# Performance work log

Measured on AMD Instinct MI355X. Metric: run time of the kernel, lower is better.

Reference implementation:

```python
import jax, jax.numpy as jnp
import numpy as np

H = 512  # hidden_dim


def setup_inputs() -> dict:
    key = jax.random.key(0)
    ks = jax.random.split(key, 9)
    B, T, TGT = 512, 512, 28
    s = 1.0 / np.sqrt(H)
    return {
        "sequence": jax.random.normal(ks[0], (B, T, 1), dtype=jnp.float32),
        "W_ih": jax.random.normal(ks[1], (4 * H, 1), dtype=jnp.float32) * s,
        "W_hh": jax.random.normal(ks[2], (4 * H, H), dtype=jnp.float32) * s,
        "b_ih": jax.random.normal(ks[3], (4 * H,), dtype=jnp.float32) * s,
        "b_hh": jax.random.normal(ks[4], (4 * H,), dtype=jnp.float32) * s,
        "fc1_w": jax.random.normal(ks[5], (H // 2, H), dtype=jnp.float32) * s,
        "fc1_b": jax.random.normal(ks[6], (H // 2,), dtype=jnp.float32) * s,
        "fc2_w": jax.random.normal(ks[7], (TGT, H // 2), dtype=jnp.float32) * (1.0 / np.sqrt(H // 2)),
        "fc2_b": jax.random.normal(ks[8], (TGT,), dtype=jnp.float32) * (1.0 / np.sqrt(H // 2)),
    }


def reference(sequence, W_ih, W_hh, b_ih, b_hh, fc1_w, fc1_b, fc2_w, fc2_b):
    B = sequence.shape[0]
    # Precompute input projections for all timesteps: [B,T,1] @ [1,4H] -> [T,B,4H]
    x_proj = jnp.einsum('bti,gi->tbg', sequence, W_ih) + b_ih + b_hh  # fold both biases

    def step(carry, xp):
        h, c = carry
        gates = xp + h @ W_hh.T                      # [B,4H]
        i, f, g, o = jnp.split(gates, 4, axis=-1)    # PyTorch LSTMCell gate order
        i = jax.nn.sigmoid(i)
        f = jax.nn.sigmoid(f)
        g = jnp.tanh(g)
        o = jax.nn.sigmoid(o)
        c_new = f * c + i * g
        h_new = o * jnp.tanh(c_new)
        return (h_new, c_new), None

    h0 = jnp.zeros((B, H), dtype=sequence.dtype)
    (h, _), _ = jax.lax.scan(step, (h0, h0), x_proj)

    # MLP head: Linear -> ReLU -> Linear, then unsqueeze to [B, target, 1]
    z = jax.nn.relu(h @ fc1_w.T + fc1_b)
    out = z @ fc2_w.T + fc2_b
    return out[:, :, None]
```

## Files before the change

kernel.cpp:

```cpp
#include <hip/hip_runtime.h>
#include <math.h>

#define H   512
#define B   512
#define T   512
#define TGT 28

typedef __bf16 bf16x8 __attribute__((ext_vector_type(8)));
typedef float  f32x4  __attribute__((ext_vector_type(4)));
typedef unsigned short u16;

#define OFF_WPH  0x000000u
#define OFF_WPL  0x200000u
#define OFF_HHI0 0x400000u
#define OFF_HLO0 0x480000u
#define OFF_SYNC 0x500000u
#define OFF_HHI1 0x501000u
#define OFF_HLO1 0x581000u

#define SMEM_BYTES 131072

__device__ inline u16 f2bf(float x) {
    unsigned u = __builtin_bit_cast(unsigned, x);
    u += 0x7FFFu + ((u >> 16) & 1u);
    return (u16)(u >> 16);
}
__device__ inline float bf2f(u16 h) {
    unsigned u = ((unsigned)h) << 16;
    return __builtin_bit_cast(float, u);
}
__device__ inline float frcp(float x) {
    float r = __builtin_amdgcn_rcpf(x);
    return r * fmaf(-x, r, 2.0f);
}
__device__ inline float fsig(float x) {
    return frcp(1.0f + __expf(-x));
}
__device__ inline float ftanh(float x) {
    return fmaf(2.0f, fsig(2.0f * x), -1.0f);
}

__device__ inline void group_barrier(int* gb, int kh, int l, int seq) {
    if (l == 0)
        __hip_atomic_store(&gb[kh], seq, __ATOMIC_RELEASE,
                           __HIP_MEMORY_SCOPE_WORKGROUP);
    int guard = 0;
    for (;;) {
        int v = __hip_atomic_load(&gb[l & 3], __ATOMIC_ACQUIRE,
                                  __HIP_MEMORY_SCOPE_WORKGROUP);
        if (__all(v >= seq)) break;
        if (++guard > (1 << 17)) break;
    }
}

__global__ __launch_bounds__(256) void init_pack(const float* __restrict__ Whh,
                                                 u16* __restrict__ wph,
                                                 u16* __restrict__ wpl) {
    int idx = blockIdx.x * 256 + threadIdx.x;
    int l  = idx & 63;
    int S  = (idx >> 6) & 15;
    int q  = (idx >> 10) & 3;
    int r  = idx >> 12;
    int g  = q * 512 + r * 16 + (l & 15);
    int k  = S * 32 + ((l >> 4) * 8);
    const float* src = Whh + (size_t)g * H + k;
    __align__(16) u16 hi8[8];
    __align__(16) u16 lo8[8];
#pragma unroll
    for (int j = 0; j < 8; ++j) {
        float w = src[j];
        u16 hb = f2bf(w);
        hi8[j] = hb;
        lo8[j] = f2bf(w - bf2f(hb));
    }
    *(uint4*)(wph + (size_t)idx * 8) = *(const uint4*)hi8;
    *(uint4*)(wpl + (size_t)idx * 8) = *(const uint4*)lo8;
}

__global__ __launch_bounds__(256) void init_state(unsigned* __restrict__ zbase) {
    int idx = blockIdx.x * 256 + threadIdx.x;
    if (idx < 263168) zbase[idx] = 0u;
}

__global__ __launch_bounds__(512, 1) void lstm_persistent(
    const u16* __restrict__ wph, const u16* __restrict__ wpl,
    u16* __restrict__ hhi0, u16* __restrict__ hlo0,
    u16* __restrict__ hhi1, u16* __restrict__ hlo1,
    int* __restrict__ sync, const float* __restrict__ seq,
    const float* __restrict__ Wih, const float* __restrict__ bih,
    const float* __restrict__ bhh)
{
    extern __shared__ char smem[];
    u16* wh = (u16*)smem;
    u16* wl = wh + 32768;
    __shared__ __align__(16) float gatesT[2][64][36];
    __shared__ int gbar[2][4];
    __shared__ int grel[2];
    __shared__ int sh_pr[2];

    const int tid = threadIdx.x;
    const int l   = tid & 63;
    const int w   = tid >> 6;
    const int g   = w >> 2;
    const int kh  = w & 3;

    if (tid == 0) {
        unsigned xcc;
        asm volatile("s_getreg_b32 %0, hwreg(HW_REG_XCC_ID)" : "=s"(xcc));
        int p = (int)(xcc & 7u);
        int r = __hip_atomic_fetch_add(&sync[p * 32], 1,
                                       __ATOMIC_RELAXED, __HIP_MEMORY_SCOPE_AGENT);
        sh_pr[0] = p;
        sh_pr[1] = r & 31;
    }
    if (tid < 8) gbar[tid >> 2][tid & 3] = 0;
    if (tid < 2) grel[tid] = 0;
    __syncthreads();
    const int p = sh_pr[0];
    const int r = sh_pr[1];
    int* arrp = &sync[256 + p * 64 + g * 32];
    int* gb   = gbar[g];

    {
        const uint4* gh = (const uint4*)(wph + (size_t)r * 32768);
        const uint4* gl = (const uint4*)(wpl + (size_t)r * 32768);
        uint4* sh = (uint4*)wh;
        uint4* sl = (uint4*)wl;
#pragma unroll
        for (int i = 0; i < 8; ++i) {
            int idx = tid + i * 512;
            sh[idx] = gh[idx];
            sl[idx] = gl[idx];
        }
    }

    const int lt   = tid & 255;
    const int cc   = lt & 15;
    const int m0   = lt >> 4;
    const int kcol = r * 16 + cc;
    float wib[4], bb[4];
#pragma unroll
    for (int q = 0; q < 4; ++q) {
        int gg = q * 512 + kcol;
        wib[q] = Wih[gg];
        bb[q]  = bih[gg] + bhh[gg];
    }
    float cr0 = 0.0f, cr1 = 0.0f;
    const int pb = p * 64;
    const int b0 = pb + g * 32 + m0;
    const int b1 = b0 + 16;

    const int arow0 = (pb + g * 32 + (l & 15)) * H;
    const int arow1 = arow0 + 16 * H;

    __syncthreads();

    for (int t = 0; t < T; ++t) {
        const u16* hih = (t & 1) ? hhi1 : hhi0;
        const u16* hil = (t & 1) ? hlo1 : hlo0;
        u16* hoh = (t & 1) ? hhi0 : hhi1;
        u16* hol = (t & 1) ? hlo0 : hlo1;

        float sv0 = seq[(size_t)b0 * T + t];
        float sv1 = seq[(size_t)b1 * T + t];

        f32x4 acc[2][4] = {};

#pragma unroll 1
        for (int s = 0; s < 4; ++s) {
            const int S  = kh * 4 + s;
            const int ka = S * 32 + ((l >> 4) * 8);
            bf16x8 a0h = *(const bf16x8*)(hih + arow0 + ka);
            bf16x8 a1h = *(const bf16x8*)(hih + arow1 + ka);
            bf16x8 a0l = *(const bf16x8*)(hil + arow0 + ka);
            bf16x8 a1l = *(const bf16x8*)(hil + arow1 + ka);
#pragma unroll
            for (int n = 0; n < 4; ++n) {
                const int fo = ((n * 16 + S) * 64 + l) * 8;
                bf16x8 bh = *(const bf16x8*)(wh + fo);
                bf16x8 bl = *(const bf16x8*)(wl + fo);
                acc[0][n] = __builtin_amdgcn_mfma_f32_16x16x32_bf16(a0h, bh, acc[0][n], 0, 0, 0);
                acc[1][n] = __builtin_amdgcn_mfma_f32_16x16x32_bf16(a1h, bh, acc[1][n], 0, 0, 0);
                acc[0][n] = __builtin_amdgcn_mfma_f32_16x16x32_bf16(a0h, bl, acc[0][n], 0, 0, 0);
                acc[1][n] = __builtin_amdgcn_mfma_f32_16x16x32_bf16(a1h, bl, acc[1][n], 0, 0, 0);
                acc[0][n] = __builtin_amdgcn_mfma_f32_16x16x32_bf16(a0l, bh, acc[0][n], 0, 0, 0);
                acc[1][n] = __builtin_amdgcn_mfma_f32_16x16x32_bf16(a1l, bh, acc[1][n], 0, 0, 0);
            }
        }

        const int base = t * 5;
#pragma unroll
        for (int rr = 0; rr < 4; ++rr) {
            if (kh == rr) {
#pragma unroll
                for (int ms = 0; ms < 2; ++ms)
#pragma unroll
                    for (int n = 0; n < 4; ++n) {
                        const int n2 = n * 16 + (l & 15);
                        const int mb = ms * 16 + ((l >> 4) << 2);
                        float* gp = &gatesT[g][n2][mb];
                        if (rr == 0) {
                            *(f32x4*)gp = acc[ms][n];
                        } else {
                            f32x4 v = *(const f32x4*)gp;
                            v += acc[ms][n];
                            *(f32x4*)gp = v;
                        }
                    }
            }
            group_barrier(gb, kh, l, base + rr + 1);
        }

        {
            float pre[4];
#pragma unroll
            for (int q = 0; q < 4; ++q) pre[q] = gatesT[g][q * 16 + cc][m0] + fmaf(sv0, wib[q], bb[q]);
            float ig = fsig(pre[0]);
            float fg = fsig(pre[1]);
            float gg2 = ftanh(pre[2]);
            float og = fsig(pre[3]);
            cr0 = fg * cr0 + ig * gg2;
            float hv = og * ftanh(cr0);
            u16 hb = f2bf(hv);
            size_t ci = (size_t)b0 * H + kcol;
            hoh[ci] = hb;
            hol[ci] = f2bf(hv - bf2f(hb));
        }
        {
            float pre[4];
#pragma unroll
            for (int q = 0; q < 4; ++q) pre[q] = gatesT[g][q * 16 + cc][m0 + 16] + fmaf(sv1, wib[q], bb[q]);
            float ig = fsig(pre[0]);
            float fg = fsig(pre[1]);
            float gg2 = ftanh(pre[2]);
            float og = fsig(pre[3]);
            cr1 = fg * cr1 + ig * gg2;
            float hv = og * ftanh(cr1);
            u16 hb = f2bf(hv);
            size_t ci = (size_t)b1 * H + kcol;
            hoh[ci] = hb;
            hol[ci] = f2bf(hv - bf2f(hb));
        }

        if (t < T - 1) {
            asm volatile("s_waitcnt vmcnt(0)" ::: "memory");
            group_barrier(gb, kh, l, base + 5);
            if (kh == 0 && l == 0) {
                __hip_atomic_fetch_add(arrp, 1, __ATOMIC_RELAXED,
                                       __HIP_MEMORY_SCOPE_AGENT);
                const int target = 32 * (t + 1);
                int guard = 0;
                while (__hip_atomic_load(arrp, __ATOMIC_RELAXED,
                                         __HIP_MEMORY_SCOPE_AGENT) < target) {
                    __builtin_amdgcn_s_sleep(1);
                    if (++guard > (1 << 18)) break;
                }
                __hip_atomic_store(&grel[g], t + 1, __ATOMIC_RELEASE,
                                   __HIP_MEMORY_SCOPE_WORKGROUP);
            }
            {
                int guard = 0;
                while (__hip_atomic_load(&grel[g], __ATOMIC_ACQUIRE,
                                         __HIP_MEMORY_SCOPE_WORKGROUP) < t + 1) {
                    if (++guard > (1 << 17)) break;
                }
            }
            asm volatile("buffer_inv sc0" ::: "memory");
        }
    }
}

__global__ __launch_bounds__(256) void head_kernel(const u16* __restrict__ hhi,
                                                   const u16* __restrict__ hlo,
                                                   const float* __restrict__ fc1w,
                                                   const float* __restrict__ fc1b,
                                                   const float* __restrict__ fc2w,
                                                   const float* __restrict__ fc2b,
                                                   float* __restrict__ out) {
    const int b = blockIdx.x;
    const int tid = threadIdx.x;
    __shared__ __align__(16) float hb[H];
    __shared__ float z[256];

    hb[tid]       = bf2f(hhi[(size_t)b * H + tid])       + bf2f(hlo[(size_t)b * H + tid]);
    hb[tid + 256] = bf2f(hhi[(size_t)b * H + tid + 256]) + bf2f(hlo[(size_t)b * H + tid + 256]);
    __syncthreads();

    float acc = fc1b[tid];
    const float4* wr = (const float4*)(fc1w + (size_t)tid * H);
    const float4* hr = (const float4*)hb;
#pragma unroll 4
    for (int kk = 0; kk < H / 4; ++kk) {
        float4 wv = wr[kk], hv = hr[kk];
        acc += wv.x * hv.x + wv.y * hv.y + wv.z * hv.z + wv.w * hv.w;
    }
    z[tid] = fmaxf(acc, 0.0f);
    __syncthreads();

    if (tid < TGT) {
        float a = fc2b[tid];
        const float* w2 = fc2w + (size_t)tid * 256;
#pragma unroll 8
        for (int j = 0; j < 256; ++j) a += z[j] * w2[j];
        out[(size_t)b * TGT + tid] = a;
    }
}

extern "C" void kernel_launch(void* const* d_in, const int* in_sizes, int n_in,
                              void* d_out, int out_size, void* d_ws, size_t ws_size,
                              hipStream_t stream) {
    const float* seq  = (const float*)d_in[0];
    const float* Wih  = (const float*)d_in[1];
    const float* Whh  = (const float*)d_in[2];
    const float* bih  = (const float*)d_in[3];
    const float* bhh  = (const float*)d_in[4];
    const float* fc1w = (const float*)d_in[5];
    const float* fc1b = (const float*)d_in[6];
    const float* fc2w = (const float*)d_in[7];
    const float* fc2b = (const float*)d_in[8];
    float* out = (float*)d_out;

    char* wsb = (char*)d_ws;
    u16* wph  = (u16*)(wsb + OFF_WPH);
    u16* wpl  = (u16*)(wsb + OFF_WPL);
    u16* hhi0 = (u16*)(wsb + OFF_HHI0);
    u16* hlo0 = (u16*)(wsb + OFF_HLO0);
    u16* hhi1 = (u16*)(wsb + OFF_HHI1);
    u16* hlo1 = (u16*)(wsb + OFF_HLO1);
    int* sync = (int*)(wsb + OFF_SYNC);

    init_pack<<<512, 256, 0, stream>>>(Whh, wph, wpl);
    init_state<<<1028, 256, 0, stream>>>((unsigned*)(wsb + OFF_HHI0));

    hipFuncSetAttribute((const void*)lstm_persistent,
                        hipFuncAttributeMaxDynamicSharedMemorySize, SMEM_BYTES);

    void* args[] = {(void*)&wph, (void*)&wpl, (void*)&hhi0, (void*)&hlo0,
                    (void*)&hhi1, (void*)&hlo1, (void*)&sync, (void*)&seq,
                    (void*)&Wih, (void*)&bih, (void*)&bhh};
    hipLaunchCooperativeKernel((const void*)lstm_persistent, dim3(256), dim3(512),
                               args, SMEM_BYTES, stream);

    head_kernel<<<B, 256, 0, stream>>>(hhi0, hlo0, fc1w, fc1b, fc2w, fc2b, out);
}
```

Measured before the change: 4.181 ms.

## Regroup warps into four batch groups with two-way K split

Warps are reorganized from 2 batch groups of 32 rows, each with a 4-way K split, into 4 groups of 16 rows, each with a 2-way K split. The per-step reduction of partial gates in shared memory drops from four serialized accumulate phases with 5 group barriers to two phases with 3 barriers. This shortens the serial sync chain inside each recurrent step. In exchange, each weight fragment read from LDS feeds only one row tile instead of two, so LDS weight traffic per warp doubles. The global cross-block arrival counters are re-indexed for the four groups.

New measurement: 12.35 ms. 195% more time.

```diff
diff --git a/kernel.cpp b/kernel.cpp
--- a/kernel.cpp
+++ b/kernel.cpp
@@ -40,13 +40,13 @@
     return fmaf(2.0f, fsig(2.0f * x), -1.0f);
 }
 
-__device__ inline void group_barrier(int* gb, int kh, int l, int seq) {
+__device__ inline void group_barrier2(int* gb, int kk, int l, int seq) {
     if (l == 0)
-        __hip_atomic_store(&gb[kh], seq, __ATOMIC_RELEASE,
+        __hip_atomic_store(&gb[kk], seq, __ATOMIC_RELEASE,
                            __HIP_MEMORY_SCOPE_WORKGROUP);
     int guard = 0;
     for (;;) {
-        int v = __hip_atomic_load(&gb[l & 3], __ATOMIC_ACQUIRE,
+        int v = __hip_atomic_load(&gb[l & 1], __ATOMIC_ACQUIRE,
                                   __HIP_MEMORY_SCOPE_WORKGROUP);
         if (__all(v >= seq)) break;
         if (++guard > (1 << 17)) break;
@@ -93,16 +93,16 @@
     extern __shared__ char smem[];
     u16* wh = (u16*)smem;
     u16* wl = wh + 32768;
-    __shared__ __align__(16) float gatesT[2][64][36];
-    __shared__ int gbar[2][4];
-    __shared__ int grel[2];
+    __shared__ __align__(16) float gatesT[4][64][20];
+    __shared__ int gbar[4][2];
+    __shared__ int grel[4];
     __shared__ int sh_pr[2];
 
     const int tid = threadIdx.x;
     const int l   = tid & 63;
     const int w   = tid >> 6;
-    const int g   = w >> 2;
-    const int kh  = w & 3;
+    const int g   = w >> 1;
+    const int kk  = w & 1;
 
     if (tid == 0) {
         unsigned xcc;
@@ -113,12 +113,12 @@
         sh_pr[0] = p;
         sh_pr[1] = r & 31;
     }
-    if (tid < 8) gbar[tid >> 2][tid & 3] = 0;
-    if (tid < 2) grel[tid] = 0;
+    if (tid < 8) gbar[tid >> 1][tid & 1] = 0;
+    if (tid < 4) grel[tid] = 0;
     __syncthreads();
     const int p = sh_pr[0];
     const int r = sh_pr[1];
-    int* arrp = &sync[256 + p * 64 + g * 32];
+    int* arrp = &sync[256 + p * 64 + g * 16];
     int* gb   = gbar[g];
 
     {
@@ -134,7 +134,7 @@
         }
     }
 
-    const int lt   = tid & 255;
+    const int lt   = tid & 127;
     const int cc   = lt & 15;
     const int m0   = lt >> 4;
     const int kcol = r * 16 + cc;
@@ -147,11 +147,10 @@
     }
     float cr0 = 0.0f, cr1 = 0.0f;
     const int pb = p * 64;
-    const int b0 = pb + g * 32 + m0;
-    const int b1 = b0 + 16;
-
-    const int arow0 = (pb + g * 32 + (l & 15)) * H;
-    const int arow1 = arow0 + 16 * H;
+    const int b0 = pb + g * 16 + m0;
+    const int b1 = b0 + 8;
+
+    const int arow0 = (pb + g * 16 + (l & 15)) * H;
 
     __syncthreads();
 
@@ -164,52 +163,47 @@
         float sv0 = seq[(size_t)b0 * T + t];
         float sv1 = seq[(size_t)b1 * T + t];
 
-        f32x4 acc[2][4] = {};
+        f32x4 acc[4] = {};
 
 #pragma unroll 1
-        for (int s = 0; s < 4; ++s) {
-            const int S  = kh * 4 + s;
+        for (int s = 0; s < 8; ++s) {
+            const int S  = kk * 8 + s;
             const int ka = S * 32 + ((l >> 4) * 8);
-            bf16x8 a0h = *(const bf16x8*)(hih + arow0 + ka);
-            bf16x8 a1h = *(const bf16x8*)(hih + arow1 + ka);
-            bf16x8 a0l = *(const bf16x8*)(hil + arow0 + ka);
-            bf16x8 a1l = *(const bf16x8*)(hil + arow1 + ka);
+            bf16x8 ah = *(const bf16x8*)(hih + arow0 + ka);
+            bf16x8 al = *(const bf16x8*)(hil + arow0 + ka);
 #pragma unroll
             for (int n = 0; n < 4; ++n) {
                 const int fo = ((n * 16 + S) * 64 + l) * 8;
                 bf16x8 bh = *(const bf16x8*)(wh + fo);
                 bf16x8 bl = *(const bf16x8*)(wl + fo);
-                acc[0][n] = __builtin_amdgcn_mfma_f32_16x16x32_bf16(a0h, bh, acc[0][n], 0, 0, 0);
-                acc[1][n] = __builtin_amdgcn_mfma_f32_16x16x32_bf16(a1h, bh, acc[1][n], 0, 0, 0);
-                acc[0][n] = __builtin_amdgcn_mfma_f32_16x16x32_bf16(a0h, bl, acc[0][n], 0, 0, 0);
-                acc[1][n] = __builtin_amdgcn_mfma_f32_16x16x32_bf16(a1h, bl, acc[1][n], 0, 0, 0);
-                acc[0][n] = __builtin_amdgcn_mfma_f32_16x16x32_bf16(a0l, bh, acc[0][n], 0, 0, 0);
-                acc[1][n] = __builtin_amdgcn_mfma_f32_16x16x32_bf16(a1l, bh, acc[1][n], 0, 0, 0);
-            }
-        }
-
-        const int base = t * 5;
-#pragma unroll
-        for (int rr = 0; rr < 4; ++rr) {
-            if (kh == rr) {
-#pragma unroll
-                for (int ms = 0; ms < 2; ++ms)
-#pragma unroll
-                    for (int n = 0; n < 4; ++n) {
-                        const int n2 = n * 16 + (l & 15);
-                        const int mb = ms * 16 + ((l >> 4) << 2);
-                        float* gp = &gatesT[g][n2][mb];
-                        if (rr == 0) {
-                            *(f32x4*)gp = acc[ms][n];
-                        } else {
-                            f32x4 v = *(const f32x4*)gp;
-                            v += acc[ms][n];
-                            *(f32x4*)gp = v;
-                        }
-                    }
-            }
-            group_barrier(gb, kh, l, base + rr + 1);
-        }
+                acc[n] = __builtin_amdgcn_mfma_f32_16x16x32_bf16(ah, bh, acc[n], 0, 0, 0);
+                acc[n] = __builtin_amdgcn_mfma_f32_16x16x32_bf16(ah, bl, acc[n], 0, 0, 0);
+                acc[n] = __builtin_amdgcn_mfma_f32_16x16x32_bf16(al, bh, acc[n], 0, 0, 0);
+            }
+        }
+
+        const int base = t * 3;
+        if (kk == 0) {
+#pragma unroll
+            for (int n = 0; n < 4; ++n) {
+                const int n2 = n * 16 + (l & 15);
+                const int mb = (l >> 4) << 2;
+                *(f32x4*)&gatesT[g][n2][mb] = acc[n];
+            }
+        }
+        group_barrier2(gb, kk, l, base + 1);
+        if (kk == 1) {
+#pragma unroll
+            for (int n = 0; n < 4; ++n) {
+                const int n2 = n * 16 + (l & 15);
+                const int mb = (l >> 4) << 2;
+                float* gp = &gatesT[g][n2][mb];
+                f32x4 v = *(const f32x4*)gp;
+                v += acc[n];
+                *(f32x4*)gp = v;
+            }
+        }
+        group_barrier2(gb, kk, l, base + 2);
 
         {
             float pre[4];
@@ -229,7 +223,7 @@
         {
             float pre[4];
 #pragma unroll
-            for (int q = 0; q < 4; ++q) pre[q] = gatesT[g][q * 16 + cc][m0 + 16] + fmaf(sv1, wib[q], bb[q]);
+            for (int q = 0; q < 4; ++q) pre[q] = gatesT[g][q * 16 + cc][m0 + 8] + fmaf(sv1, wib[q], bb[q]);
             float ig = fsig(pre[0]);
             float fg = fsig(pre[1]);
             float gg2 = ftanh(pre[2]);
@@ -244,8 +238,8 @@
 
         if (t < T - 1) {
             asm volatile("s_waitcnt vmcnt(0)" ::: "memory");
-            group_barrier(gb, kh, l, base + 5);
-            if (kh == 0 && l == 0) {
+            group_barrier2(gb, kk, l, base + 3);
+            if (kk == 0 && l == 0) {
                 __hip_atomic_fetch_add(arrp, 1, __ATOMIC_RELAXED,
                                        __HIP_MEMORY_SCOPE_AGENT);
                 const int target = 32 * (t + 1);
```

## Read low weight half from global, halve gate-reduction barriers, add sleep in spin

Applied to the files above, without the earlier changes.

Only the high bf16 half of the recurrent weights is staged into LDS. The low half is now read from global memory (L2/L1) on every timestep, which halves dynamic shared memory. The four-way sequential gate reduction over k-slices is replaced by two accumulation buffers written in pairs, cutting per-step group barriers from five to three. The intra-block spin wait also gets an s_sleep to reduce contention. The tradeoff is that global loads inside the MFMA inner loop may add latency on every step.

New measurement: 5.007 ms. +19.8%, slower.

```diff
diff --git a/kernel.cpp b/kernel.cpp
--- a/kernel.cpp
+++ b/kernel.cpp
@@ -18,7 +18,7 @@
 #define OFF_HHI1 0x501000u
 #define OFF_HLO1 0x581000u
 
-#define SMEM_BYTES 131072
+#define SMEM_BYTES 65536
 
 __device__ inline u16 f2bf(float x) {
     unsigned u = __builtin_bit_cast(unsigned, x);
@@ -92,8 +92,8 @@
 {
     extern __shared__ char smem[];
     u16* wh = (u16*)smem;
-    u16* wl = wh + 32768;
-    __shared__ __align__(16) float gatesT[2][64][36];
+    __shared__ __align__(16) float gA[2][64][36];
+    __shared__ __align__(16) float gB[2][64][36];
     __shared__ int gbar[2][4];
     __shared__ int grel[2];
     __shared__ int sh_pr[2];
@@ -123,16 +123,14 @@
 
     {
         const uint4* gh = (const uint4*)(wph + (size_t)r * 32768);
-        const uint4* gl = (const uint4*)(wpl + (size_t)r * 32768);
         uint4* sh = (uint4*)wh;
-        uint4* sl = (uint4*)wl;
 #pragma unroll
         for (int i = 0; i < 8; ++i) {
             int idx = tid + i * 512;
             sh[idx] = gh[idx];
-            sl[idx] = gl[idx];
-        }
-    }
+        }
+    }
+    const u16* glo = wpl + (size_t)r * 32768;
 
     const int lt   = tid & 255;
     const int cc   = lt & 15;
@@ -178,7 +176,7 @@
             for (int n = 0; n < 4; ++n) {
                 const int fo = ((n * 16 + S) * 64 + l) * 8;
                 bf16x8 bh = *(const bf16x8*)(wh + fo);
-                bf16x8 bl = *(const bf16x8*)(wl + fo);
+                bf16x8 bl = *(const bf16x8*)(glo + fo);
                 acc[0][n] = __builtin_amdgcn_mfma_f32_16x16x32_bf16(a0h, bh, acc[0][n], 0, 0, 0);
                 acc[1][n] = __builtin_amdgcn_mfma_f32_16x16x32_bf16(a1h, bh, acc[1][n], 0, 0, 0);
                 acc[0][n] = __builtin_amdgcn_mfma_f32_16x16x32_bf16(a0h, bl, acc[0][n], 0, 0, 0);
@@ -188,33 +186,41 @@
             }
         }
 
-        const int base = t * 5;
-#pragma unroll
-        for (int rr = 0; rr < 4; ++rr) {
-            if (kh == rr) {
-#pragma unroll
-                for (int ms = 0; ms < 2; ++ms)
-#pragma unroll
-                    for (int n = 0; n < 4; ++n) {
-                        const int n2 = n * 16 + (l & 15);
-                        const int mb = ms * 16 + ((l >> 4) << 2);
-                        float* gp = &gatesT[g][n2][mb];
-                        if (rr == 0) {
-                            *(f32x4*)gp = acc[ms][n];
-                        } else {
-                            f32x4 v = *(const f32x4*)gp;
-                            v += acc[ms][n];
-                            *(f32x4*)gp = v;
-                        }
-                    }
-            }
-            group_barrier(gb, kh, l, base + rr + 1);
-        }
+        const int base = t * 3;
+        if (kh == 0 || kh == 2) {
+            float (*gt)[36] = (kh == 0) ? gA[g] : gB[g];
+#pragma unroll
+            for (int ms = 0; ms < 2; ++ms)
+#pragma unroll
+                for (int n = 0; n < 4; ++n) {
+                    const int n2 = n * 16 + (l & 15);
+                    const int mb = ms * 16 + ((l >> 4) << 2);
+                    *(f32x4*)&gt[n2][mb] = acc[ms][n];
+                }
+        }
+        group_barrier(gb, kh, l, base + 1);
+        if (kh == 1 || kh == 3) {
+            float (*gt)[36] = (kh == 1) ? gA[g] : gB[g];
+#pragma unroll
+            for (int ms = 0; ms < 2; ++ms)
+#pragma unroll
+                for (int n = 0; n < 4; ++n) {
+                    const int n2 = n * 16 + (l & 15);
+                    const int mb = ms * 16 + ((l >> 4) << 2);
+                    float* gp = &gt[n2][mb];
+                    f32x4 v = *(const f32x4*)gp;
+                    v += acc[ms][n];
+                    *(f32x4*)gp = v;
+                }
+        }
+        group_barrier(gb, kh, l, base + 2);
 
         {
             float pre[4];
 #pragma unroll
-            for (int q = 0; q < 4; ++q) pre[q] = gatesT[g][q * 16 + cc][m0] + fmaf(sv0, wib[q], bb[q]);
+            for (int q = 0; q < 4; ++q)
+                pre[q] = gA[g][q * 16 + cc][m0] + gB[g][q * 16 + cc][m0]
+                       + fmaf(sv0, wib[q], bb[q]);
             float ig = fsig(pre[0]);
             float fg = fsig(pre[1]);
             float gg2 = ftanh(pre[2]);
@@ -229,7 +235,9 @@
         {
             float pre[4];
 #pragma unroll
-            for (int q = 0; q < 4; ++q) pre[q] = gatesT[g][q * 16 + cc][m0 + 16] + fmaf(sv1, wib[q], bb[q]);
+            for (int q = 0; q < 4; ++q)
+                pre[q] = gA[g][q * 16 + cc][m0 + 16] + gB[g][q * 16 + cc][m0 + 16]
+                       + fmaf(sv1, wib[q], bb[q]);
             float ig = fsig(pre[0]);
             float fg = fsig(pre[1]);
             float gg2 = ftanh(pre[2]);
@@ -244,7 +252,7 @@
 
         if (t < T - 1) {
             asm volatile("s_waitcnt vmcnt(0)" ::: "memory");
-            group_barrier(gb, kh, l, base + 5);
+            group_barrier(gb, kh, l, base + 3);
             if (kh == 0 && l == 0) {
                 __hip_atomic_fetch_add(arrp, 1, __ATOMIC_RELAXED,
                                        __HIP_MEMORY_SCOPE_AGENT);
@@ -262,7 +270,8 @@
                 int guard = 0;
                 while (__hip_atomic_load(&grel[g], __ATOMIC_ACQUIRE,
                                          __HIP_MEMORY_SCOPE_WORKGROUP) < t + 1) {
-                    if (++guard > (1 << 17)) break;
+                    __builtin_amdgcn_s_sleep(2);
+                    if (++guard > (1 << 16)) break;
                 }
             }
             asm volatile("buffer_inv sc0" ::: "memory");
```

## Split LSTM gate GEMM across waves by K-half and N-half to cut reduction barriers

Applied to the files above, without the earlier changes.

Each of the four waves in a batch group previously computed all four N-tiles over one quarter of K, then reduced through shared memory in four serialized barrier rounds. Now waves split work two ways in K and two ways in N, so the reduction needs only two barrier rounds per timestep. Each wave now loads the A fragments over twice as many K steps, adding some global reads of h. Spin-wait guard limits are also lowered, which risks breaking out early if a barrier wait runs long.

New measurement: 5.756 ms. 1.38x slower.

```diff
diff --git a/kernel.cpp b/kernel.cpp
--- a/kernel.cpp
+++ b/kernel.cpp
@@ -40,16 +40,16 @@
     return fmaf(2.0f, fsig(2.0f * x), -1.0f);
 }
 
-__device__ inline void group_barrier(int* gb, int kh, int l, int seq) {
+__device__ inline void group_barrier(int* gb, int wq, int l, int seq) {
     if (l == 0)
-        __hip_atomic_store(&gb[kh], seq, __ATOMIC_RELEASE,
+        __hip_atomic_store(&gb[wq], seq, __ATOMIC_RELEASE,
                            __HIP_MEMORY_SCOPE_WORKGROUP);
     int guard = 0;
     for (;;) {
         int v = __hip_atomic_load(&gb[l & 3], __ATOMIC_ACQUIRE,
                                   __HIP_MEMORY_SCOPE_WORKGROUP);
         if (__all(v >= seq)) break;
-        if (++guard > (1 << 17)) break;
+        if (++guard > (1 << 14)) break;
     }
 }
 
@@ -102,7 +102,9 @@
     const int l   = tid & 63;
     const int w   = tid >> 6;
     const int g   = w >> 2;
-    const int kh  = w & 3;
+    const int wq  = w & 3;
+    const int kk  = wq & 1;
+    const int nn  = wq >> 1;
 
     if (tid == 0) {
         unsigned xcc;
@@ -164,52 +166,57 @@
         float sv0 = seq[(size_t)b0 * T + t];
         float sv1 = seq[(size_t)b1 * T + t];
 
-        f32x4 acc[2][4] = {};
+        f32x4 acc[2][2] = {};
 
 #pragma unroll 1
-        for (int s = 0; s < 4; ++s) {
-            const int S  = kh * 4 + s;
+        for (int s = 0; s < 8; ++s) {
+            const int S  = kk * 8 + s;
             const int ka = S * 32 + ((l >> 4) * 8);
             bf16x8 a0h = *(const bf16x8*)(hih + arow0 + ka);
             bf16x8 a1h = *(const bf16x8*)(hih + arow1 + ka);
             bf16x8 a0l = *(const bf16x8*)(hil + arow0 + ka);
             bf16x8 a1l = *(const bf16x8*)(hil + arow1 + ka);
 #pragma unroll
-            for (int n = 0; n < 4; ++n) {
+            for (int j = 0; j < 2; ++j) {
+                const int n  = nn * 2 + j;
                 const int fo = ((n * 16 + S) * 64 + l) * 8;
                 bf16x8 bh = *(const bf16x8*)(wh + fo);
                 bf16x8 bl = *(const bf16x8*)(wl + fo);
-                acc[0][n] = __builtin_amdgcn_mfma_f32_16x16x32_bf16(a0h, bh, acc[0][n], 0, 0, 0);
-                acc[1][n] = __builtin_amdgcn_mfma_f32_16x16x32_bf16(a1h, bh, acc[1][n], 0, 0, 0);
-                acc[0][n] = __builtin_amdgcn_mfma_f32_16x16x32_bf16(a0h, bl, acc[0][n], 0, 0, 0);
-                acc[1][n] = __builtin_amdgcn_mfma_f32_16x16x32_bf16(a1h, bl, acc[1][n], 0, 0, 0);
-                acc[0][n] = __builtin_amdgcn_mfma_f32_16x16x32_bf16(a0l, bh, acc[0][n], 0, 0, 0);
-                acc[1][n] = __builtin_amdgcn_mfma_f32_16x16x32_bf16(a1l, bh, acc[1][n], 0, 0, 0);
+                acc[0][j] = __builtin_amdgcn_mfma_f32_16x16x32_bf16(a0h, bh, acc[0][j], 0, 0, 0);
+                acc[1][j] = __builtin_amdgcn_mfma_f32_16x16x32_bf16(a1h, bh, acc[1][j], 0, 0, 0);
+                acc[0][j] = __builtin_amdgcn_mfma_f32_16x16x32_bf16(a0h, bl, acc[0][j], 0, 0, 0);
+                acc[1][j] = __builtin_amdgcn_mfma_f32_16x16x32_bf16(a1h, bl, acc[1][j], 0, 0, 0);
+                acc[0][j] = __builtin_amdgcn_mfma_f32_16x16x32_bf16(a0l, bh, acc[0][j], 0, 0, 0);
+                acc[1][j] = __builtin_amdgcn_mfma_f32_16x16x32_bf16(a1l, bh, acc[1][j], 0, 0, 0);
             }
         }
 
-        const int base = t * 5;
-#pragma unroll
-        for (int rr = 0; rr < 4; ++rr) {
-            if (kh == rr) {
-#pragma unroll
-                for (int ms = 0; ms < 2; ++ms)
-#pragma unroll
-                    for (int n = 0; n < 4; ++n) {
-                        const int n2 = n * 16 + (l & 15);
-                        const int mb = ms * 16 + ((l >> 4) << 2);
-                        float* gp = &gatesT[g][n2][mb];
-                        if (rr == 0) {
-                            *(f32x4*)gp = acc[ms][n];
-                        } else {
-                            f32x4 v = *(const f32x4*)gp;
-                            v += acc[ms][n];
-                            *(f32x4*)gp = v;
-                        }
-                    }
-            }
-            group_barrier(gb, kh, l, base + rr + 1);
-        }
+        const int base = t * 3;
+        if (kk == 0) {
+#pragma unroll
+            for (int ms = 0; ms < 2; ++ms)
+#pragma unroll
+                for (int j = 0; j < 2; ++j) {
+                    const int n2 = (nn * 2 + j) * 16 + (l & 15);
+                    const int mb = ms * 16 + ((l >> 4) << 2);
+                    *(f32x4*)&gatesT[g][n2][mb] = acc[ms][j];
+                }
+        }
+        group_barrier(gb, wq, l, base + 1);
+        if (kk == 1) {
+#pragma unroll
+            for (int ms = 0; ms < 2; ++ms)
+#pragma unroll
+                for (int j = 0; j < 2; ++j) {
+                    const int n2 = (nn * 2 + j) * 16 + (l & 15);
+                    const int mb = ms * 16 + ((l >> 4) << 2);
+                    float* gp = &gatesT[g][n2][mb];
+                    f32x4 v = *(const f32x4*)gp;
+                    v += acc[ms][j];
+                    *(f32x4*)gp = v;
+                }
+        }
+        group_barrier(gb, wq, l, base + 2);
 
         {
             float pre[4];
@@ -244,8 +251,8 @@
 
         if (t < T - 1) {
             asm volatile("s_waitcnt vmcnt(0)" ::: "memory");
-            group_barrier(gb, kh, l, base + 5);
-            if (kh == 0 && l == 0) {
+            group_barrier(gb, wq, l, base + 3);
+            if (wq == 0 && l == 0) {
                 __hip_atomic_fetch_add(arrp, 1, __ATOMIC_RELAXED,
                                        __HIP_MEMORY_SCOPE_AGENT);
                 const int target = 32 * (t + 1);
@@ -253,7 +260,7 @@
                 while (__hip_atomic_load(arrp, __ATOMIC_RELAXED,
                                          __HIP_MEMORY_SCOPE_AGENT) < target) {
                     __builtin_amdgcn_s_sleep(1);
-                    if (++guard > (1 << 18)) break;
+                    if (++guard > (1 << 15)) break;
                 }
                 __hip_atomic_store(&grel[g], t + 1, __ATOMIC_RELEASE,
                                    __HIP_MEMORY_SCOPE_WORKGROUP);
@@ -262,7 +269,7 @@
                 int guard = 0;
                 while (__hip_atomic_load(&grel[g], __ATOMIC_ACQUIRE,
                                          __HIP_MEMORY_SCOPE_WORKGROUP) < t + 1) {
-                    if (++guard > (1 << 17)) break;
+                    if (++guard > (1 << 14)) break;
                 }
             }
             asm volatile("buffer_inv sc0" ::: "memory");
```
